# Optimization experiments

Measured on AMD Instinct MI355X. Metric: run time of the kernel, lower is better.

Reference implementation:

```python
import jax, jax.numpy as jnp
import numpy as np

N_NODES = 50000
N_EDGES = 400000
D_IN = 128
D_H = 128
N_CLASSES = 20
N_GRAPHS = 256
EPS_BN = 1e-5


def _lin_params(key, d_in, d_out, scale=0.05):
    kw, kb = jax.random.split(key)
    W = jax.random.normal(kw, (d_in, d_out), jnp.float32) * scale
    b = jax.random.normal(kb, (d_out,), jnp.float32) * scale
    return W, b


def setup_inputs() -> dict:
    key = jax.random.key(0)
    ks = jax.random.split(key, 20)
    inp = {
        "x": jax.random.normal(ks[0], (N_NODES, D_IN), jnp.float32),
        "edge_index": jax.random.randint(ks[1], (2, N_EDGES), 0, N_NODES, jnp.int32),
        "batch": jnp.sort(jax.random.randint(ks[2], (N_NODES,), 0, N_GRAPHS, jnp.int32)),
    }
    kidx = 3
    for li, d_in in zip((1, 2, 3), (D_IN, D_H, D_H)):
        for nm in ("q", "k", "v", "s"):
            W, b = _lin_params(ks[kidx], d_in, D_H)
            kidx += 1
            inp[f"W{nm}{li}"] = W
            inp[f"b{nm}{li}"] = b
        inp[f"gamma{li}"] = jnp.ones((D_H,), jnp.float32)
        inp[f"beta{li}"] = jnp.zeros((D_H,), jnp.float32)
    Wl, bl = _lin_params(ks[kidx], D_H, N_CLASSES)
    inp["Wlin"] = Wl
    inp["blin"] = bl
    return inp


def _segment_softmax(logits, seg, n):
    m = jax.ops.segment_max(logits, seg, num_segments=n)
    e = jnp.exp(logits - m[seg])
    s = jax.ops.segment_sum(e, seg, num_segments=n)
    return e / (s[seg] + 1e-16)


def _transformer_conv(x, src, dst, Wq, bq, Wk, bk, Wv, bv, Ws, bs):
    # heads=1, concat=True, root_weight=True (PyG TransformerConv defaults)
    q = x @ Wq + bq  # [N, d]
    k = x @ Wk + bk
    v = x @ Wv + bv
    d = q.shape[-1]
    logits = jnp.sum(q[dst] * k[src], axis=-1) / jnp.sqrt(jnp.float32(d))  # [E]
    alpha = _segment_softmax(logits, dst, x.shape[0])
    out = jax.ops.segment_sum(alpha[:, None] * v[src], dst, num_segments=x.shape[0])
    return out + x @ Ws + bs


def _batch_norm(x, gamma, beta):
    mu = jnp.mean(x, axis=0)
    var = jnp.var(x, axis=0)
    return gamma * (x - mu) * jax.lax.rsqrt(var + EPS_BN) + beta


def _global_mean_pool(x, batch, n_graphs):
    sums = jax.ops.segment_sum(x, batch, num_segments=n_graphs)
    cnt = jax.ops.segment_sum(jnp.ones((x.shape[0],), x.dtype), batch, num_segments=n_graphs)
    return sums / jnp.maximum(cnt, 1.0)[:, None]


def reference(x, edge_index, batch,
              Wq1, bq1, Wk1, bk1, Wv1, bv1, Ws1, bs1, gamma1, beta1,
              Wq2, bq2, Wk2, bk2, Wv2, bv2, Ws2, bs2, gamma2, beta2,
              Wq3, bq3, Wk3, bk3, Wv3, bv3, Ws3, bs3, gamma3, beta3,
              Wlin, blin):
    src, dst = edge_index[0], edge_index[1]
    h = _transformer_conv(x, src, dst, Wq1, bq1, Wk1, bk1, Wv1, bv1, Ws1, bs1)
    h = jax.nn.relu(_batch_norm(h, gamma1, beta1))  # dropout inactive (eval)
    h = _transformer_conv(h, src, dst, Wq2, bq2, Wk2, bk2, Wv2, bv2, Ws2, bs2)
    h = jax.nn.relu(_batch_norm(h, gamma2, beta2))
    h = _transformer_conv(h, src, dst, Wq3, bq3, Wk3, bk3, Wv3, bv3, Ws3, bs3)
    h = jax.nn.relu(_batch_norm(h, gamma3, beta3))
    g = _global_mean_pool(h, batch, N_GRAPHS)  # [G, d]
    return g @ Wlin + blin  # [G, num_classes]
```

## Files before the change

kernel.cpp:

```cpp
#include <hip/hip_runtime.h>

#define N_NODES 50000
#define N_EDGES 400000
#define DH 128
#define N_GRAPHS 256

#define SCAN_CHUNK 512
#define N_CHUNKS ((N_NODES + SCAN_CHUNK - 1) / SCAN_CHUNK)
#define ATTN_BLOCKS ((N_NODES + 7) / 8)

typedef __bf16 bf16x8 __attribute__((ext_vector_type(8)));
typedef float f32x4 __attribute__((ext_vector_type(4)));
typedef _Float16 f16x4 __attribute__((ext_vector_type(4)));

#define DEV __device__ __forceinline__

DEV unsigned short f2bf(float f) {
  union { float f; unsigned int i; } v; v.f = f;
  unsigned int x = v.i;
  unsigned int r = (x + 0x7fffu + ((x >> 16) & 1u)) >> 16;
  return (unsigned short)r;
}

struct WPtrs { const float* w[12]; };

__global__ void repack_kernel(WPtrs wp, unsigned short* __restrict__ WB) {
  int mat = blockIdx.y;
  int m = blockIdx.x * 256 + threadIdx.x;
  int j = m & 7;
  int lane = (m >> 3) & 63;
  int ct = (m >> 9) & 7;
  int kk = m >> 12;
  int i = kk * 32 + (lane >> 4) * 8 + j;
  int o = ct * 16 + (lane & 15);
  WB[mat * 16384 + m] = f2bf(wp.w[mat][i * 128 + o]);
}

__global__ void f32_to_bf16(const float* __restrict__ in, unsigned short* __restrict__ out,
                            int total4) {
  int i = blockIdx.x * 256 + threadIdx.x;
  if (i >= total4) return;
  float4 v = *reinterpret_cast<const float4*>(in + i * 4);
  ushort4 o;
  o.x = f2bf(v.x); o.y = f2bf(v.y); o.z = f2bf(v.z); o.w = f2bf(v.w);
  *reinterpret_cast<ushort4*>(out + i * 4) = o;
}

__global__ void deg_count(const int* __restrict__ ei, int* __restrict__ deg, int E) {
  int e = blockIdx.x * 256 + threadIdx.x;
  if (e < E) atomicAdd(&deg[ei[E + e]], 1);
}

__global__ __launch_bounds__(256) void scan_sum(const int* __restrict__ deg,
                                                int* __restrict__ partials, int N) {
  __shared__ int red[256];
  int b = blockIdx.x, t = threadIdx.x;
  int base = b * SCAN_CHUNK + t * 2;
  int s = 0;
  if (base + 1 < N) { int2 v = *reinterpret_cast<const int2*>(deg + base); s = v.x + v.y; }
  else if (base < N) s = deg[base];
  red[t] = s;
  __syncthreads();
  for (int off = 128; off; off >>= 1) {
    if (t < off) red[t] += red[t + off];
    __syncthreads();
  }
  if (t == 0) partials[b] = red[0];
}

__global__ __launch_bounds__(128) void scan_partials(int* __restrict__ partials) {
  __shared__ int s[128];
  int t = threadIdx.x;
  int v = (t < N_CHUNKS) ? partials[t] : 0;
  s[t] = v;
  __syncthreads();
  for (int off = 1; off < 128; off <<= 1) {
    int o = (t >= off) ? s[t - off] : 0;
    __syncthreads();
    s[t] += o;
    __syncthreads();
  }
  if (t < N_CHUNKS) partials[t] = s[t] - v;
}

__global__ __launch_bounds__(256) void scan_apply(const int* __restrict__ deg,
                                                  const int* __restrict__ partials,
                                                  int* __restrict__ rowptr,
                                                  int* __restrict__ cursor, int N, int E) {
  __shared__ int s[256];
  int b = blockIdx.x, t = threadIdx.x;
  int base = b * SCAN_CHUNK + t * 2;
  int d0 = 0, d1 = 0;
  if (base + 1 < N) { int2 v = *reinterpret_cast<const int2*>(deg + base); d0 = v.x; d1 = v.y; }
  else if (base < N) d0 = deg[base];
  int local = d0 + d1;
  s[t] = local;
  __syncthreads();
  for (int off = 1; off < 256; off <<= 1) {
    int o = (t >= off) ? s[t - off] : 0;
    __syncthreads();
    s[t] += o;
    __syncthreads();
  }
  int offp = partials[b] + s[t] - local;
  if (base < N)     { rowptr[base] = offp;          cursor[base] = offp; }
  if (base + 1 < N) { rowptr[base + 1] = offp + d0; cursor[base + 1] = offp + d0; }
  if (b == 0 && t == 0) rowptr[N] = E;
}

__global__ void csr_scatter(const int* __restrict__ ei, int* __restrict__ cursor,
                            int* __restrict__ adj, int E) {
  int e = blockIdx.x * 256 + threadIdx.x;
  if (e < E) {
    int dst = ei[E + e];
    int pos = atomicAdd(&cursor[dst], 1);
    adj[pos] = ei[e];
  }
}

struct GemmOut { void* Y[4]; const float* bias[4]; };

#define LDP 136

__global__ __launch_bounds__(256) void gemm_proj(
    const unsigned short* __restrict__ X,
    const float* __restrict__ Hin,
    const float* __restrict__ scale, const float* __restrict__ shift,
    const unsigned short* __restrict__ WB4,
    GemmOut go, int useBN, int N)
{
  __shared__ __align__(16) unsigned short xs[64 * LDP];

  const int t = threadIdx.x;
  const int rowBase = blockIdx.x * 64;
  const int igc = (t & 15) * 8;

  if (useBN) {
    float4 sc0 = *reinterpret_cast<const float4*>(scale + igc);
    float4 sc1 = *reinterpret_cast<const float4*>(scale + igc + 4);
    float4 sh0 = *reinterpret_cast<const float4*>(shift + igc);
    float4 sh1 = *reinterpret_cast<const float4*>(shift + igc + 4);
#pragma unroll
    for (int j = 0; j < 4; ++j) {
      int v = t + 256 * j;
      int r = v >> 4;
      int grow = rowBase + r;
      ushort4 o0 = make_ushort4(0, 0, 0, 0), o1 = make_ushort4(0, 0, 0, 0);
      if (grow < N) {
        float4 a = *reinterpret_cast<const float4*>(Hin + (size_t)grow * 128 + igc);
        float4 b = *reinterpret_cast<const float4*>(Hin + (size_t)grow * 128 + igc + 4);
        o0.x = f2bf(fmaxf(a.x * sc0.x + sh0.x, 0.f));
        o0.y = f2bf(fmaxf(a.y * sc0.y + sh0.y, 0.f));
        o0.z = f2bf(fmaxf(a.z * sc0.z + sh0.z, 0.f));
        o0.w = f2bf(fmaxf(a.w * sc0.w + sh0.w, 0.f));
        o1.x = f2bf(fmaxf(b.x * sc1.x + sh1.x, 0.f));
        o1.y = f2bf(fmaxf(b.y * sc1.y + sh1.y, 0.f));
        o1.z = f2bf(fmaxf(b.z * sc1.z + sh1.z, 0.f));
        o1.w = f2bf(fmaxf(b.w * sc1.w + sh1.w, 0.f));
      }
      *reinterpret_cast<ushort4*>(&xs[r * LDP + igc]) = o0;
      *reinterpret_cast<ushort4*>(&xs[r * LDP + igc + 4]) = o1;
    }
  } else {
#pragma unroll
    for (int j = 0; j < 4; ++j) {
      int v = t + 256 * j;
      int r = v >> 4;
      int grow = rowBase + r;
      uint4 val = make_uint4(0u, 0u, 0u, 0u);
      if (grow < N) val = *reinterpret_cast<const uint4*>(X + (size_t)grow * 128 + igc);
      *reinterpret_cast<uint4*>(&xs[r * LDP + igc]) = val;
    }
  }
  __syncthreads();

  const int wave = t >> 6;
  const int lane = t & 63;
  const int ln16 = lane & 15;
  const int quad = lane >> 4;
  const int r0 = wave * 16;

  bf16x8 afrag[4];
#pragma unroll
  for (int kk = 0; kk < 4; ++kk)
    afrag[kk] = *reinterpret_cast<const bf16x8*>(&xs[(r0 + ln16) * LDP + kk * 32 + quad * 8]);

  for (int proj = 0; proj < 4; ++proj) {
    const unsigned short* __restrict__ WB = WB4 + proj * 16384;
    const float* __restrict__ bias = go.bias[proj];

    f32x4 acc[8] = {};
#pragma unroll
    for (int kk = 0; kk < 4; ++kk) {
#pragma unroll
      for (int ct = 0; ct < 8; ++ct) {
        bf16x8 b = *reinterpret_cast<const bf16x8*>(WB + ((kk * 8 + ct) * 64 + lane) * 8);
        acc[ct] = __builtin_amdgcn_mfma_f32_16x16x32_bf16(afrag[kk], b, acc[ct], 0, 0, 0);
      }
    }

    const bool asHalf = (proj < 3);
    float* __restrict__ Yf = (float*)go.Y[proj];
    _Float16* __restrict__ Yh = (_Float16*)go.Y[proj];

#pragma unroll
    for (int ct = 0; ct < 8; ++ct) {
      int col = ct * 16 + ln16;
      float bv = bias[col];
#pragma unroll
      for (int reg = 0; reg < 4; ++reg) {
        int grow = rowBase + r0 + quad * 4 + reg;
        if (grow < N) {
          float v = acc[ct][reg] + bv;
          if (asHalf) Yh[(size_t)grow * 128 + col] = (_Float16)v;
          else        Yf[(size_t)grow * 128 + col] = v;
        }
      }
    }
  }
}

__global__ __launch_bounds__(256) void node_attn(
    const int* __restrict__ rowptr, const int* __restrict__ adj,
    const _Float16* __restrict__ Q, const _Float16* __restrict__ K,
    const _Float16* __restrict__ V, float* __restrict__ H,
    float* __restrict__ Pbuf, int N)
{
  __shared__ float lsum[8][128];
  __shared__ float lsq[8][128];
  int t = threadIdx.x;
  int w = t >> 5, lane = t & 31;
  int n = blockIdx.x * 8 + w;
  bool valid = n < N;
  int nn = valid ? n : 0;
  int p0 = 0, p1 = 0;
  if (valid) { p0 = rowptr[n]; p1 = rowptr[n + 1]; }

  f16x4 qh = *reinterpret_cast<const f16x4*>(Q + (size_t)nn * 128 + lane * 4);
  float4 q = make_float4((float)qh.x, (float)qh.y, (float)qh.z, (float)qh.w);
  float m = -INFINITY, s = 0.f;
  float4 acc = make_float4(0.f, 0.f, 0.f, 0.f);

  int p = p0;
  for (; p + 1 < p1; p += 2) {
    int s0 = adj[p], s1 = adj[p + 1];
    f16x4 k0 = *reinterpret_cast<const f16x4*>(K + (size_t)s0 * 128 + lane * 4);
    f16x4 k1 = *reinterpret_cast<const f16x4*>(K + (size_t)s1 * 128 + lane * 4);
    float d0 = q.x * (float)k0.x + q.y * (float)k0.y + q.z * (float)k0.z + q.w * (float)k0.w;
    float d1 = q.x * (float)k1.x + q.y * (float)k1.y + q.z * (float)k1.z + q.w * (float)k1.w;
#pragma unroll
    for (int off = 16; off; off >>= 1) {
      d0 += __shfl_xor(d0, off, 32);
      d1 += __shfl_xor(d1, off, 32);
    }
    float l0 = d0 * 0.08838834764831845f;
    float l1 = d1 * 0.08838834764831845f;
    float mn = fmaxf(m, fmaxf(l0, l1));
    float sc = __expf(m - mn);
    float w0 = __expf(l0 - mn);
    float w1 = __expf(l1 - mn);
    f16x4 v0 = *reinterpret_cast<const f16x4*>(V + (size_t)s0 * 128 + lane * 4);
    f16x4 v1 = *reinterpret_cast<const f16x4*>(V + (size_t)s1 * 128 + lane * 4);
    acc.x = acc.x * sc + w0 * (float)v0.x + w1 * (float)v1.x;
    acc.y = acc.y * sc + w0 * (float)v0.y + w1 * (float)v1.y;
    acc.z = acc.z * sc + w0 * (float)v0.z + w1 * (float)v1.z;
    acc.w = acc.w * sc + w0 * (float)v0.w + w1 * (float)v1.w;
    s = s * sc + w0 + w1;
    m = mn;
  }
  if (p < p1) {
    int s0 = adj[p];
    f16x4 k0 = *reinterpret_cast<const f16x4*>(K + (size_t)s0 * 128 + lane * 4);
    float d0 = q.x * (float)k0.x + q.y * (float)k0.y + q.z * (float)k0.z + q.w * (float)k0.w;
#pragma unroll
    for (int off = 16; off; off >>= 1) d0 += __shfl_xor(d0, off, 32);
    float l0 = d0 * 0.08838834764831845f;
    float mn = fmaxf(m, l0);
    float sc = __expf(m - mn);
    float w0 = __expf(l0 - mn);
    f16x4 v0 = *reinterpret_cast<const f16x4*>(V + (size_t)s0 * 128 + lane * 4);
    acc.x = acc.x * sc + w0 * (float)v0.x;
    acc.y = acc.y * sc + w0 * (float)v0.y;
    acc.z = acc.z * sc + w0 * (float)v0.z;
    acc.w = acc.w * sc + w0 * (float)v0.w;
    s = s * sc + w0;
    m = mn;
  }

  float4 h = make_float4(0.f, 0.f, 0.f, 0.f);
  if (valid) {
    float inv = 1.0f / (s + 1e-16f);
    h = *reinterpret_cast<const float4*>(H + (size_t)n * 128 + lane * 4);
    h.x += acc.x * inv;
    h.y += acc.y * inv;
    h.z += acc.z * inv;
    h.w += acc.w * inv;
    *reinterpret_cast<float4*>(H + (size_t)n * 128 + lane * 4) = h;
  }

  *reinterpret_cast<float4*>(&lsum[w][lane * 4]) = h;
  float4 h2 = make_float4(h.x * h.x, h.y * h.y, h.z * h.z, h.w * h.w);
  *reinterpret_cast<float4*>(&lsq[w][lane * 4]) = h2;
  __syncthreads();

  int f = t & 127;
  float a = 0.f;
  if (t < 128) {
#pragma unroll
    for (int n8 = 0; n8 < 8; ++n8) a += lsum[n8][f];
  } else {
#pragma unroll
    for (int n8 = 0; n8 < 8; ++n8) a += lsq[n8][f];
  }
  Pbuf[(size_t)blockIdx.x * 256 + t] = a;
}

__global__ __launch_bounds__(256) void bn_reduceA(const float* __restrict__ Pbuf,
                                                  float* __restrict__ partial) {
  int t = threadIdx.x;
  float s0 = 0.f, s1 = 0.f, s2 = 0.f, s3 = 0.f;
  int r = blockIdx.x;
  for (; r + 192 < ATTN_BLOCKS; r += 256) {
    s0 += Pbuf[(size_t)(r      ) * 256 + t];
    s1 += Pbuf[(size_t)(r +  64) * 256 + t];
    s2 += Pbuf[(size_t)(r + 128) * 256 + t];
    s3 += Pbuf[(size_t)(r + 192) * 256 + t];
  }
  for (; r < ATTN_BLOCKS; r += 64) s0 += Pbuf[(size_t)r * 256 + t];
  partial[blockIdx.x * 256 + t] = s0 + s1 + s2 + s3;
}

__global__ __launch_bounds__(256) void bn_reduceB(
    const float* __restrict__ partial,
    const float* __restrict__ gamma, const float* __restrict__ beta,
    float* __restrict__ scale, float* __restrict__ shift, int N)
{
  __shared__ float red[256];
  int t = threadIdx.x;
  float s0 = 0.f, s1 = 0.f, s2 = 0.f, s3 = 0.f;
#pragma unroll
  for (int r = 0; r < 64; r += 4) {
    s0 += partial[(r + 0) * 256 + t];
    s1 += partial[(r + 1) * 256 + t];
    s2 += partial[(r + 2) * 256 + t];
    s3 += partial[(r + 3) * 256 + t];
  }
  red[t] = s0 + s1 + s2 + s3;
  __syncthreads();
  if (t < 128) {
    float mean = red[t] / (float)N;
    float var = red[t + 128] / (float)N - mean * mean;
    var = fmaxf(var, 0.f);
    float sc = gamma[t] * rsqrtf(var + 1e-5f);
    scale[t] = sc;
    shift[t] = beta[t] - mean * sc;
  }
}

__global__ __launch_bounds__(256) void pool_linear(
    const float* __restrict__ H, const float* __restrict__ scale,
    const float* __restrict__ shift, const int* __restrict__ batch,
    const float* __restrict__ Wlin, const float* __restrict__ blin,
    float* __restrict__ out, int N)
{
  __shared__ float red[256];
  __shared__ float pool[128];
  int g = blockIdx.x;
  int t = threadIdx.x;

  int lo = 0, hi = N;
  while (lo < hi) { int mid = (lo + hi) >> 1; if (batch[mid] < g) lo = mid + 1; else hi = mid; }
  int start = lo;
  hi = N;
  while (lo < hi) { int mid = (lo + hi) >> 1; if (batch[mid] < g + 1) lo = mid + 1; else hi = mid; }
  int end = lo;
  int cnt = end - start;

  int f = t & 127, half = t >> 7;
  float sc = scale[f], sh = shift[f];
  float s = 0.f;
  for (int row = start + half; row < end; row += 2)
    s += fmaxf(H[(size_t)row * 128 + f] * sc + sh, 0.f);
  red[t] = s;
  __syncthreads();
  if (t < 128)
    pool[t] = (red[t] + red[t + 128]) / fmaxf((float)cnt, 1.f);
  __syncthreads();

  if (t < 20) {
    float acc = 0.f;
#pragma unroll 4
    for (int i = 0; i < 128; ++i)
      acc += pool[i] * Wlin[i * 20 + t];
    out[g * 20 + t] = acc + blin[t];
  }
}

extern "C" void kernel_launch(void* const* d_in, const int* in_sizes, int n_in,
                              void* d_out, int out_size, void* d_ws, size_t ws_size,
                              hipStream_t stream)
{
  const int N = N_NODES, E = N_EDGES, G = N_GRAPHS;

  const float* x = (const float*)d_in[0];
  const int* ei = (const int*)d_in[1];
  const int* batch = (const int*)d_in[2];
  const float* Wlin = (const float*)d_in[33];
  const float* blin = (const float*)d_in[34];

  char* ws = (char*)d_ws;
  size_t off = 0;
  auto alloc = [&](size_t bytes) -> void* {
    void* p = ws + off;
    off = (off + bytes + 255) & ~(size_t)255;
    return p;
  };
  unsigned short* WB = (unsigned short*)alloc(12 * 16384 * sizeof(unsigned short));
  _Float16* Qh  = (_Float16*)alloc((size_t)N * 128 * 2);
  _Float16* Kh  = (_Float16*)alloc((size_t)N * 128 * 2);
  _Float16* Vh  = (_Float16*)alloc((size_t)N * 128 * 2);
  float* H      = (float*)alloc((size_t)N * 128 * 4);
  int* deg      = (int*)alloc((size_t)N * 4);
  int* rowptr   = (int*)alloc((size_t)(N + 1) * 4);
  int* cursor   = (int*)alloc((size_t)N * 4);
  int* adj      = (int*)alloc((size_t)E * 4);
  int* partials = (int*)alloc((size_t)N_CHUNKS * 4);
  float* Pbuf   = (float*)alloc((size_t)ATTN_BLOCKS * 256 * 4);
  float* bnpart = (float*)alloc((size_t)64 * 256 * 4);
  float* scale  = (float*)alloc(128 * 4);
  float* shift  = (float*)alloc(128 * 4);
  unsigned short* Xb = (unsigned short*)alloc((size_t)N * 128 * 2);

  WPtrs wp;
  for (int L = 0; L < 3; ++L) {
    wp.w[L * 4 + 0] = (const float*)d_in[3 + L * 10 + 0];
    wp.w[L * 4 + 1] = (const float*)d_in[3 + L * 10 + 2];
    wp.w[L * 4 + 2] = (const float*)d_in[3 + L * 10 + 4];
    wp.w[L * 4 + 3] = (const float*)d_in[3 + L * 10 + 6];
  }
  repack_kernel<<<dim3(64, 12), 256, 0, stream>>>(wp, WB);
  f32_to_bf16<<<(N * 128 / 4 + 255) / 256, 256, 0, stream>>>(x, Xb, N * 128 / 4);

  hipMemsetAsync(deg, 0, (size_t)N * 4, stream);
  deg_count<<<(E + 255) / 256, 256, 0, stream>>>(ei, deg, E);
  scan_sum<<<N_CHUNKS, 256, 0, stream>>>(deg, partials, N);
  scan_partials<<<1, 128, 0, stream>>>(partials);
  scan_apply<<<N_CHUNKS, 256, 0, stream>>>(deg, partials, rowptr, cursor, N, E);
  csr_scatter<<<(E + 255) / 256, 256, 0, stream>>>(ei, cursor, adj, E);

  for (int L = 0; L < 3; ++L) {
    GemmOut go;
    go.Y[0] = Qh; go.Y[1] = Kh; go.Y[2] = Vh; go.Y[3] = H;
    go.bias[0] = (const float*)d_in[3 + L * 10 + 1];
    go.bias[1] = (const float*)d_in[3 + L * 10 + 3];
    go.bias[2] = (const float*)d_in[3 + L * 10 + 5];
    go.bias[3] = (const float*)d_in[3 + L * 10 + 7];
    gemm_proj<<<(N + 63) / 64, 256, 0, stream>>>(
        Xb, H, scale, shift, WB + L * 4 * 16384, go, (L > 0) ? 1 : 0, N);

    node_attn<<<ATTN_BLOCKS, 256, 0, stream>>>(rowptr, adj, Qh, Kh, Vh, H, Pbuf, N);

    bn_reduceA<<<64, 256, 0, stream>>>(Pbuf, bnpart);
    bn_reduceB<<<1, 256, 0, stream>>>(bnpart,
        (const float*)d_in[3 + L * 10 + 8],
        (const float*)d_in[3 + L * 10 + 9],
        scale, shift, N);

    if (L == 2) {
      pool_linear<<<G, 256, 0, stream>>>(H, scale, shift, batch, Wlin, blin,
                                         (float*)d_out, N);
    }
  }
}
```

Before: 496.7 us.

## Store hidden state in fp16 and parallelize mean pooling with chunked atomics

The hidden state H (root projection plus attention output) is now stored in fp16 instead of fp32. This halves its traffic in the GEMM epilogue, in the node attention read-modify-write, in the next layer's BN input load, and in pooling. Pooling is also split into many 64-row chunk blocks that atomically add per-graph partial sums, followed by a small final linear kernel. This replaces 256 blocks that each walked a whole graph. The fp16 storage of H adds rounding error to the residual and BN path, and the atomics make the pooled sums order-dependent.

```diff
diff --git a/kernel.cpp b/kernel.cpp
--- a/kernel.cpp
+++ b/kernel.cpp
@@ -8,10 +8,12 @@
 #define SCAN_CHUNK 512
 #define N_CHUNKS ((N_NODES + SCAN_CHUNK - 1) / SCAN_CHUNK)
 #define ATTN_BLOCKS ((N_NODES + 7) / 8)
+#define POOL_CHUNKS ((N_NODES + 63) / 64)
 
 typedef __bf16 bf16x8 __attribute__((ext_vector_type(8)));
 typedef float f32x4 __attribute__((ext_vector_type(4)));
 typedef _Float16 f16x4 __attribute__((ext_vector_type(4)));
+typedef _Float16 f16x8 __attribute__((ext_vector_type(8)));
 
 #define DEV __device__ __forceinline__
 
@@ -118,13 +120,13 @@
   }
 }
 
-struct GemmOut { void* Y[4]; const float* bias[4]; };
+struct GemmOut { _Float16* Y[4]; const float* bias[4]; };
 
 #define LDP 136
 
 __global__ __launch_bounds__(256) void gemm_proj(
     const unsigned short* __restrict__ X,
-    const float* __restrict__ Hin,
+    const _Float16* __restrict__ Hin,
     const float* __restrict__ scale, const float* __restrict__ shift,
     const unsigned short* __restrict__ WB4,
     GemmOut go, int useBN, int N)
@@ -147,16 +149,15 @@
       int grow = rowBase + r;
       ushort4 o0 = make_ushort4(0, 0, 0, 0), o1 = make_ushort4(0, 0, 0, 0);
       if (grow < N) {
-        float4 a = *reinterpret_cast<const float4*>(Hin + (size_t)grow * 128 + igc);
-        float4 b = *reinterpret_cast<const float4*>(Hin + (size_t)grow * 128 + igc + 4);
-        o0.x = f2bf(fmaxf(a.x * sc0.x + sh0.x, 0.f));
-        o0.y = f2bf(fmaxf(a.y * sc0.y + sh0.y, 0.f));
-        o0.z = f2bf(fmaxf(a.z * sc0.z + sh0.z, 0.f));
-        o0.w = f2bf(fmaxf(a.w * sc0.w + sh0.w, 0.f));
-        o1.x = f2bf(fmaxf(b.x * sc1.x + sh1.x, 0.f));
-        o1.y = f2bf(fmaxf(b.y * sc1.y + sh1.y, 0.f));
-        o1.z = f2bf(fmaxf(b.z * sc1.z + sh1.z, 0.f));
-        o1.w = f2bf(fmaxf(b.w * sc1.w + sh1.w, 0.f));
+        f16x8 hv = *reinterpret_cast<const f16x8*>(Hin + (size_t)grow * 128 + igc);
+        o0.x = f2bf(fmaxf((float)hv[0] * sc0.x + sh0.x, 0.f));
+        o0.y = f2bf(fmaxf((float)hv[1] * sc0.y + sh0.y, 0.f));
+        o0.z = f2bf(fmaxf((float)hv[2] * sc0.z + sh0.z, 0.f));
+        o0.w = f2bf(fmaxf((float)hv[3] * sc0.w + sh0.w, 0.f));
+        o1.x = f2bf(fmaxf((float)hv[4] * sc1.x + sh1.x, 0.f));
+        o1.y = f2bf(fmaxf((float)hv[5] * sc1.y + sh1.y, 0.f));
+        o1.z = f2bf(fmaxf((float)hv[6] * sc1.z + sh1.z, 0.f));
+        o1.w = f2bf(fmaxf((float)hv[7] * sc1.w + sh1.w, 0.f));
       }
       *reinterpret_cast<ushort4*>(&xs[r * LDP + igc]) = o0;
       *reinterpret_cast<ushort4*>(&xs[r * LDP + igc + 4]) = o1;
@@ -199,10 +200,7 @@
       }
     }
 
-    const bool asHalf = (proj < 3);
-    float* __restrict__ Yf = (float*)go.Y[proj];
-    _Float16* __restrict__ Yh = (_Float16*)go.Y[proj];
-
+    _Float16* __restrict__ Yh = go.Y[proj];
 #pragma unroll
     for (int ct = 0; ct < 8; ++ct) {
       int col = ct * 16 + ln16;
@@ -210,11 +208,7 @@
 #pragma unroll
       for (int reg = 0; reg < 4; ++reg) {
         int grow = rowBase + r0 + quad * 4 + reg;
-        if (grow < N) {
-          float v = acc[ct][reg] + bv;
-          if (asHalf) Yh[(size_t)grow * 128 + col] = (_Float16)v;
-          else        Yf[(size_t)grow * 128 + col] = v;
-        }
+        if (grow < N) Yh[(size_t)grow * 128 + col] = (_Float16)(acc[ct][reg] + bv);
       }
     }
   }
@@ -223,7 +217,7 @@
 __global__ __launch_bounds__(256) void node_attn(
     const int* __restrict__ rowptr, const int* __restrict__ adj,
     const _Float16* __restrict__ Q, const _Float16* __restrict__ K,
-    const _Float16* __restrict__ V, float* __restrict__ H,
+    const _Float16* __restrict__ V, _Float16* __restrict__ H,
     float* __restrict__ Pbuf, int N)
 {
   __shared__ float lsum[8][128];
@@ -290,12 +284,14 @@
   float4 h = make_float4(0.f, 0.f, 0.f, 0.f);
   if (valid) {
     float inv = 1.0f / (s + 1e-16f);
-    h = *reinterpret_cast<const float4*>(H + (size_t)n * 128 + lane * 4);
-    h.x += acc.x * inv;
-    h.y += acc.y * inv;
-    h.z += acc.z * inv;
-    h.w += acc.w * inv;
-    *reinterpret_cast<float4*>(H + (size_t)n * 128 + lane * 4) = h;
+    f16x4 hh = *reinterpret_cast<const f16x4*>(H + (size_t)n * 128 + lane * 4);
+    h.x = (float)hh.x + acc.x * inv;
+    h.y = (float)hh.y + acc.y * inv;
+    h.z = (float)hh.z + acc.z * inv;
+    h.w = (float)hh.w + acc.w * inv;
+    f16x4 ho;
+    ho.x = (_Float16)h.x; ho.y = (_Float16)h.y; ho.z = (_Float16)h.z; ho.w = (_Float16)h.w;
+    *reinterpret_cast<f16x4*>(H + (size_t)n * 128 + lane * 4) = ho;
   }
 
   *reinterpret_cast<float4*>(&lsum[w][lane * 4]) = h;
@@ -357,42 +353,46 @@
   }
 }
 
-__global__ __launch_bounds__(256) void pool_linear(
-    const float* __restrict__ H, const float* __restrict__ scale,
+__global__ __launch_bounds__(256) void pool_chunk(
+    const _Float16* __restrict__ H, const float* __restrict__ scale,
     const float* __restrict__ shift, const int* __restrict__ batch,
+    float* __restrict__ pooled, int N)
+{
+  int f = threadIdx.x & 127, half = threadIdx.x >> 7;
+  int base = blockIdx.x * 64;
+  int lim = min(base + 64, N);
+  float sc = scale[f], sh = shift[f];
+  int curg = -1; float s = 0.f;
+  for (int row = base + half; row < lim; row += 2) {
+    int g = batch[row];
+    if (g != curg) {
+      if (curg >= 0) unsafeAtomicAdd(pooled + curg * 128 + f, s);
+      curg = g; s = 0.f;
+    }
+    s += fmaxf((float)H[(size_t)row * 128 + f] * sc + sh, 0.f);
+  }
+  if (curg >= 0) unsafeAtomicAdd(pooled + curg * 128 + f, s);
+}
+
+__global__ __launch_bounds__(64) void final_linear(
+    const float* __restrict__ pooled, const int* __restrict__ batch,
     const float* __restrict__ Wlin, const float* __restrict__ blin,
     float* __restrict__ out, int N)
 {
-  __shared__ float red[256];
-  __shared__ float pool[128];
   int g = blockIdx.x;
-  int t = threadIdx.x;
-
+  int c = threadIdx.x;
   int lo = 0, hi = N;
   while (lo < hi) { int mid = (lo + hi) >> 1; if (batch[mid] < g) lo = mid + 1; else hi = mid; }
   int start = lo;
   hi = N;
   while (lo < hi) { int mid = (lo + hi) >> 1; if (batch[mid] < g + 1) lo = mid + 1; else hi = mid; }
-  int end = lo;
-  int cnt = end - start;
-
-  int f = t & 127, half = t >> 7;
-  float sc = scale[f], sh = shift[f];
-  float s = 0.f;
-  for (int row = start + half; row < end; row += 2)
-    s += fmaxf(H[(size_t)row * 128 + f] * sc + sh, 0.f);
-  red[t] = s;
-  __syncthreads();
-  if (t < 128)
-    pool[t] = (red[t] + red[t + 128]) / fmaxf((float)cnt, 1.f);
-  __syncthreads();
-
-  if (t < 20) {
+  float inv = 1.0f / fmaxf((float)(lo - start), 1.f);
+  if (c < 20) {
     float acc = 0.f;
 #pragma unroll 4
     for (int i = 0; i < 128; ++i)
-      acc += pool[i] * Wlin[i * 20 + t];
-    out[g * 20 + t] = acc + blin[t];
+      acc += pooled[g * 128 + i] * Wlin[i * 20 + c];
+    out[g * 20 + c] = acc * inv + blin[c];
   }
 }
 
@@ -419,7 +419,7 @@
   _Float16* Qh  = (_Float16*)alloc((size_t)N * 128 * 2);
   _Float16* Kh  = (_Float16*)alloc((size_t)N * 128 * 2);
   _Float16* Vh  = (_Float16*)alloc((size_t)N * 128 * 2);
-  float* H      = (float*)alloc((size_t)N * 128 * 4);
+  _Float16* Hh  = (_Float16*)alloc((size_t)N * 128 * 2);
   int* deg      = (int*)alloc((size_t)N * 4);
   int* rowptr   = (int*)alloc((size_t)(N + 1) * 4);
   int* cursor   = (int*)alloc((size_t)N * 4);
@@ -429,6 +429,7 @@
   float* bnpart = (float*)alloc((size_t)64 * 256 * 4);
   float* scale  = (float*)alloc(128 * 4);
   float* shift  = (float*)alloc(128 * 4);
+  float* pooled = (float*)alloc((size_t)G * 128 * 4);
   unsigned short* Xb = (unsigned short*)alloc((size_t)N * 128 * 2);
 
   WPtrs wp;
@@ -450,15 +451,15 @@
 
   for (int L = 0; L < 3; ++L) {
     GemmOut go;
-    go.Y[0] = Qh; go.Y[1] = Kh; go.Y[2] = Vh; go.Y[3] = H;
+    go.Y[0] = Qh; go.Y[1] = Kh; go.Y[2] = Vh; go.Y[3] = Hh;
     go.bias[0] = (const float*)d_in[3 + L * 10 + 1];
     go.bias[1] = (const float*)d_in[3 + L * 10 + 3];
     go.bias[2] = (const float*)d_in[3 + L * 10 + 5];
     go.bias[3] = (const float*)d_in[3 + L * 10 + 7];
     gemm_proj<<<(N + 63) / 64, 256, 0, stream>>>(
-        Xb, H, scale, shift, WB + L * 4 * 16384, go, (L > 0) ? 1 : 0, N);
-
-    node_attn<<<ATTN_BLOCKS, 256, 0, stream>>>(rowptr, adj, Qh, Kh, Vh, H, Pbuf, N);
+        Xb, Hh, scale, shift, WB + L * 4 * 16384, go, (L > 0) ? 1 : 0, N);
+
+    node_attn<<<ATTN_BLOCKS, 256, 0, stream>>>(rowptr, adj, Qh, Kh, Vh, Hh, Pbuf, N);
 
     bn_reduceA<<<64, 256, 0, stream>>>(Pbuf, bnpart);
     bn_reduceB<<<1, 256, 0, stream>>>(bnpart,
@@ -467,8 +468,9 @@
         scale, shift, N);
 
     if (L == 2) {
-      pool_linear<<<G, 256, 0, stream>>>(H, scale, shift, batch, Wlin, blin,
-                                         (float*)d_out, N);
-    }
-  }
-}
+      hipMemsetAsync(pooled, 0, (size_t)G * 128 * 4, stream);
+      pool_chunk<<<POOL_CHUNKS, 256, 0, stream>>>(Hh, scale, shift, batch, pooled, N);
+      final_linear<<<G, 64, 0, stream>>>(pooled, batch, Wlin, blin, (float*)d_out, N);
+    }
+  }
+}
```

Result: faster. 479.7 us (-3.4%).
